# Optimization experiments

Hardware: AMD Instinct MI355X
Metric: run time of the kernel (lower is better)

Reference implementation:

```python
import jax, jax.numpy as jnp
import numpy as np

N, C, T, V, M = 256, 3, 300, 25, 2
H = 256            # sub_hidden == main_hidden
NUM_CLASS = 60
IN = C * V         # 75 = dim_point * num_joint


def _lstm(xs, Wih, Whh, bih, bhh):
    """Single-layer LSTM over (N,T,I) -> (N,T,H), zero initial state."""
    h_dim = Whh.shape[1]
    n = xs.shape[0]
    b = bih + bhh

    def step(carry, x_t):
        h, c = carry
        g = x_t @ Wih.T + h @ Whh.T + b          # (N,4H)
        i, f, gg, o = jnp.split(g, 4, axis=-1)
        c = jax.nn.sigmoid(f) * c + jax.nn.sigmoid(i) * jnp.tanh(gg)
        h = jax.nn.sigmoid(o) * jnp.tanh(c)
        return (h, c), h

    init = (jnp.zeros((n, h_dim), xs.dtype), jnp.zeros((n, h_dim), xs.dtype))
    _, hs = jax.lax.scan(step, init, jnp.swapaxes(xs, 0, 1))
    return jnp.swapaxes(hs, 0, 1)                # (N,T,H)


def _rot_mats(a):
    """Batched Rx@Ry@Rz from angles a (N,3), matching the torch formulas."""
    c, s = jnp.cos(a), jnp.sin(a)
    z = jnp.zeros_like(c[:, 0]); o = jnp.ones_like(z)
    Rx = jnp.stack([jnp.stack([o, z, z], -1),
                    jnp.stack([z,  c[:, 0], s[:, 0]], -1),
                    jnp.stack([z, -s[:, 0], c[:, 0]], -1)], -2)
    Ry = jnp.stack([jnp.stack([c[:, 1], z, -s[:, 1]], -1),
                    jnp.stack([z, o, z], -1),
                    jnp.stack([s[:, 1], z,  c[:, 1]], -1)], -2)
    Rz = jnp.stack([jnp.stack([ c[:, 2], s[:, 2], z], -1),
                    jnp.stack([-s[:, 2], c[:, 2], z], -1),
                    jnp.stack([z, z, o], -1)], -2)
    return Rx @ Ry @ Rz                           # (N,3,3)


def setup_inputs() -> dict:
    key = jax.random.key(0)
    ks = iter(jax.random.split(key, 40))
    g = lambda shape: jax.random.normal(next(ks), shape, dtype=jnp.float32) * 0.05
    inp = {"x": jax.random.normal(next(ks), (N, C, T, V, M), dtype=jnp.float32)}
    for pre, i_dim in (("rot", IN), ("tr", IN)):
        inp[pre + "_Wih"] = g((4 * H, i_dim))
        inp[pre + "_Whh"] = g((4 * H, H))
        inp[pre + "_bih"] = g((4 * H,))
        inp[pre + "_bhh"] = g((4 * H,))
        inp[pre + "_fcW"] = g((3, H))
        inp[pre + "_fcb"] = g((3,))
    for li, i_dim in ((0, IN), (1, H), (2, H)):
        inp[f"m{li}_Wih"] = g((4 * H, i_dim))
        inp[f"m{li}_Whh"] = g((4 * H, H))
        inp[f"m{li}_bih"] = g((4 * H,))
        inp[f"m{li}_bhh"] = g((4 * H,))
    inp["fcW"] = g((NUM_CLASS, H))
    inp["fcb"] = g((NUM_CLASS,))
    return inp


def reference(x,
              rot_Wih, rot_Whh, rot_bih, rot_bhh, rot_fcW, rot_fcb,
              tr_Wih, tr_Whh, tr_bih, tr_bhh, tr_fcW, tr_fcb,
              m0_Wih, m0_Whh, m0_bih, m0_bhh,
              m1_Wih, m1_Whh, m1_bih, m1_bhh,
              m2_Wih, m2_Whh, m2_bih, m2_bhh,
              fcW, fcb):
    n, c, t, v, m = x.shape

    def person_feat(xm):                          # xm: (N,C,T,V)
        seq = xm.transpose(0, 2, 1, 3).reshape(n, t, c * v)   # (N,T,CV)
        h_rot = _lstm(seq, rot_Wih, rot_Whh, rot_bih, rot_bhh)[:, -1]
        ang = (h_rot @ rot_fcW.T + rot_fcb) * jnp.pi          # (N,3)
        h_tr = _lstm(seq, tr_Wih, tr_Whh, tr_bih, tr_bhh)[:, -1]
        trans = h_tr @ tr_fcW.T + tr_fcb                      # (N,3)
        R = _rot_mats(ang)                                    # (N,3,3)
        xs = xm - trans[:, :, None, None]                     # translate
        xr = jnp.einsum('nij,njk->nik', R, xs.reshape(n, c, t * v))
        seq2 = xr.reshape(n, c, t, v).transpose(0, 2, 1, 3).reshape(n, t, c * v)
        h = _lstm(seq2, m0_Wih, m0_Whh, m0_bih, m0_bhh)
        h = _lstm(h, m1_Wih, m1_Whh, m1_bih, m1_bhh)
        h = _lstm(h, m2_Wih, m2_Whh, m2_bih, m2_bhh)
        return h[:, -1]                                       # (N,H)

    h0 = person_feat(x[..., 0])
    h1 = person_feat(x[..., 1])
    out = jnp.maximum(h0, h1)
    return out @ fcW.T + fcb                                  # (N,num_class)
```

## Files before the change

### kernel.cpp

```cpp
#include <hip/hip_runtime.h>
#include <hip/hip_fp16.h>

#define N_ 256
#define C_ 3
#define T_ 300
#define V_ 25
#define H_ 256
#define G4_ 1024
#define IN_ 75
#define XP1_ 96
#define NCLS_ 60

typedef _Float16 half_t;
typedef __attribute__((ext_vector_type(8))) _Float16 half8;
typedef __attribute__((ext_vector_type(4))) float f32x4;
typedef __attribute__((ext_vector_type(4))) unsigned int uint4v;
typedef __attribute__((ext_vector_type(2))) unsigned int uint2v;

static_assert(sizeof(half8) == 16, "half8 must be 16B");

__device__ __forceinline__ float tanh_f(float x) {
  x = fminf(fmaxf(x, -15.0f), 15.0f);
  float e = __expf(2.0f * x);
  return (e - 1.0f) / (e + 1.0f);
}

__device__ __forceinline__ half8 gload16_cc(const void* p) {
  uint4v r;
  asm volatile("global_load_dwordx4 %0, %1, off sc0 sc1" : "=v"(r) : "v"(p));
  return __builtin_bit_cast(half8, r);
}
__device__ __forceinline__ void store8_cc(void* p, uint2v v) {
  asm volatile("global_store_dwordx2 %0, %1, off sc0 sc1" :: "v"(p), "v"(v) : "memory");
}
__device__ __forceinline__ void waitvm0() {
  asm volatile("s_waitcnt vmcnt(0)" ::: "memory");
  __builtin_amdgcn_sched_barrier(0);
}

__global__ void pack_wcat(const float* __restrict__ Whh, const float* __restrict__ Wih,
                          const float* __restrict__ bih, const float* __restrict__ bhh,
                          half_t* __restrict__ dstW, float* __restrict__ dstB,
                          int inDim, int Kc) {
  int idx = blockIdx.x * 256 + threadIdx.x;
  int tot = G4_ * Kc;
  if (idx < tot) {
    int row = idx / Kc, k = idx % Kc;
    float v = 0.0f;
    if (k < H_) v = Whh[row * H_ + k];
    else if (k - H_ < inDim) v = Wih[row * inDim + (k - H_)];
    dstW[idx] = (half_t)v;
  }
  if (idx < G4_) dstB[idx] = bih[idx] + bhh[idx];
}

__global__ void pack_seq(const float* __restrict__ x, half_t* __restrict__ seqb) {
  int idx = blockIdx.x * 256 + threadIdx.x;
  const int tot = 2 * N_ * T_ * XP1_;
  if (idx >= tot) return;
  int k = idx % XP1_; int r = idx / XP1_;
  int t = r % T_; int r2 = r / T_;
  int n = r2 % N_; int p = r2 / N_;
  float v = 0.0f;
  if (k < IN_) {
    int c = k / V_, vv = k % V_;
    v = x[(((size_t)n * C_ + c) * T_ + t) * (V_ * 2) + vv * 2 + p];
  }
  seqb[idx] = (half_t)v;
}

template<int KT, bool POLLX>
__device__ __forceinline__ void run_layer(
    const half_t* __restrict__ Wcat, const float* __restrict__ bias,
    const half_t* __restrict__ xseq,
    half_t* __restrict__ ring, int rr,
    half_t* __restrict__ hseq, float* __restrict__ hlast,
    int ringRow0, int seqRow0, int u0, int member,
    half_t* hstage) {
  constexpr int XKT = KT - 8;
  constexpr int XK = XKT * 32;
  constexpr int Kc = KT * 32;
  const int tid = threadIdx.x, lane = tid & 63, wave = tid >> 6;
  const int col = lane & 15, khalf = lane >> 4, klo8 = khalf * 8, gq = col & 3;
  const int srow = tid >> 3, spart = tid & 7;

  half8 wreg[2][KT];
  float brg[2];
#pragma unroll
  for (int ntp = 0; ntp < 2; ++ntp) {
    int lrow = (wave * 2 + ntp) * 16 + col;
    int grow = (lrow & 3) * 256 + u0 + (lrow >> 2);
#pragma unroll
    for (int kt = 0; kt < KT; ++kt)
      wreg[ntp][kt] = *reinterpret_cast<const half8*>(Wcat + (size_t)grow * Kc + kt * 32 + klo8);
    brg[ntp] = bias[grow];
  }

  const half_t* xrow[2];
#pragma unroll
  for (int c = 0; c < 2; ++c)
    xrow[c] = xseq + (size_t)(seqRow0 + c * 16 + col) * T_ * XK + klo8;

  float creg[2][2][4] = {};

  auto chk = [](half8 v) -> unsigned {
    uint4v u = __builtin_bit_cast(uint4v, v);
    return ((u[0] & 0xFFFFu) == 0xFFFFu) | ((u[1] & 0xFFFFu) == 0xFFFFu) |
           ((u[2] & 0xFFFFu) == 0xFFFFu) | ((u[3] & 0xFFFFu) == 0xFFFFu);
  };

#pragma unroll 1
  for (int t = 0; t < T_; ++t) {
    const int sc_ = t % 3;
    const int sp_ = (t + 2) % 3;
    const int sn_ = (t + 1) % 3;
    const bool hasH = (t > 0);

    half8 ax[2][XKT];
    half8 ah[2][8];

    if (!POLLX) {
#pragma unroll
      for (int c = 0; c < 2; ++c)
#pragma unroll
        for (int kx = 0; kx < XKT; ++kx)
          ax[c][kx] = *reinterpret_cast<const half8*>(xrow[c] + (size_t)t * XK + kx * 32);
    }

    if (hasH || POLLX) {
      int guard = 0;
      for (;;) {
        if (hasH) {
#pragma unroll
          for (int c = 0; c < 2; ++c)
#pragma unroll
            for (int kt = 0; kt < 8; ++kt)
              ah[c][kt] = gload16_cc(
                  ring + ((size_t)(sp_ * 8 + kt) * rr + ringRow0 + c * 16 + col) * 32 + klo8);
        }
        if (POLLX) {
#pragma unroll
          for (int c = 0; c < 2; ++c)
#pragma unroll
            for (int kx = 0; kx < XKT; ++kx)
              ax[c][kx] = gload16_cc(xrow[c] + (size_t)t * XK + kx * 32);
        }
        waitvm0();
        unsigned bad = 0;
        if (hasH) {
#pragma unroll
          for (int c = 0; c < 2; ++c)
#pragma unroll
            for (int kt = 0; kt < 8; ++kt) bad |= chk(ah[c][kt]);
        }
        if (POLLX) {
#pragma unroll
          for (int c = 0; c < 2; ++c)
#pragma unroll
            for (int kx = 0; kx < XKT; ++kx) bad |= chk(ax[c][kx]);
        }
        if (__all(bad == 0u)) break;
        if (++guard > (1 << 20)) break;
        __builtin_amdgcn_s_sleep(1);
      }
      __syncthreads();
      __builtin_amdgcn_sched_barrier(0);
    }

    {
      uint2v sent = {0xFFFFFFFFu, 0xFFFFFFFFu};
      store8_cc(ring + ((size_t)(sn_ * 8 + member) * rr + ringRow0 + srow) * 32 + spart * 4, sent);
    }

#pragma unroll
    for (int c = 0; c < 2; ++c) {
      f32x4 acc[2];
      acc[0] = (f32x4){brg[0], brg[0], brg[0], brg[0]};
      acc[1] = (f32x4){brg[1], brg[1], brg[1], brg[1]};
      if (hasH) {
#pragma unroll
        for (int kt = 0; kt < 8; ++kt) {
          acc[0] = __builtin_amdgcn_mfma_f32_16x16x32_f16(ah[c][kt], wreg[0][kt], acc[0], 0, 0, 0);
          acc[1] = __builtin_amdgcn_mfma_f32_16x16x32_f16(ah[c][kt], wreg[1][kt], acc[1], 0, 0, 0);
        }
      }
#pragma unroll
      for (int kx = 0; kx < XKT; ++kx) {
        acc[0] = __builtin_amdgcn_mfma_f32_16x16x32_f16(ax[c][kx], wreg[0][8 + kx], acc[0], 0, 0, 0);
        acc[1] = __builtin_amdgcn_mfma_f32_16x16x32_f16(ax[c][kx], wreg[1][8 + kx], acc[1], 0, 0, 0);
      }
#pragma unroll
      for (int ntp = 0; ntp < 2; ++ntp) {
        int nt = wave * 2 + ntp;
        int ul = nt * 4 + (col >> 2);
#pragma unroll
        for (int r = 0; r < 4; ++r) {
          float v = acc[ntp][r];
          float y = (gq == 2) ? 2.0f * v : v;
          float s = 1.0f / (1.0f + __expf(-y));
          float av = (gq == 2) ? (2.0f * s - 1.0f) : s;
          float b1v = __shfl_xor(av, 1);
          float b2v = __shfl_xor(av, 2);
          float b3v = __shfl_xor(b1v, 2);
          auto pick = [&](int k2) { return k2 == 0 ? av : (k2 == 1 ? b1v : (k2 == 2 ? b2v : b3v)); };
          float iv = pick(gq), fv = pick(gq ^ 1), gv = pick(gq ^ 2), ov = pick(gq ^ 3);
          float cc = fv * creg[c][ntp][r] + iv * gv;
          creg[c][ntp][r] = cc;
          float h = ov * tanh_f(cc);
          if (gq == 0) {
            int s_ = c * 16 + khalf * 4 + r;
            hstage[s_ * 32 + ul] = (half_t)h;
            if (hlast != nullptr && t == T_ - 1)
              hlast[(size_t)(seqRow0 + s_) * H_ + u0 + ul] = h;
          }
        }
      }
    }
    __syncthreads();

    waitvm0();
    {
      uint2v val = *reinterpret_cast<const uint2v*>(&hstage[srow * 32 + spart * 4]);
      store8_cc(ring + ((size_t)(sc_ * 8 + member) * rr + ringRow0 + srow) * 32 + spart * 4, val);
      if (hseq)
        store8_cc(&hseq[((size_t)(seqRow0 + srow) * T_ + t) * H_ + u0 + spart * 4], val);
    }
  }
}

__global__ __launch_bounds__(256, 1) void lstm_p1(
    const half_t* __restrict__ W0, const half_t* __restrict__ W1,
    const float* __restrict__ b0, const float* __restrict__ b1,
    const half_t* __restrict__ xseq, half_t* __restrict__ ring,
    float* __restrict__ hl0, float* __restrict__ hl1) {
  __shared__ __align__(8) half_t hstage[32 * 32];
  const int member = blockIdx.x >> 5;
  const int g = blockIdx.x & 31;
  const int run = g >> 4;
  run_layer<11, false>(run ? W1 : W0, run ? b1 : b0, xseq,
                       ring, 1024, nullptr, run ? hl1 : hl0,
                       g * 32, g * 32 - run * 512, member * 32, member, hstage);
}

template<int KT, bool POLLX>
__device__ __forceinline__ void ml_layer(
    const half_t* __restrict__ Wcat, const float* __restrict__ bias,
    const half_t* __restrict__ xseq,
    half_t* __restrict__ ring,
    half_t* __restrict__ hseq, float* __restrict__ hlast,
    unsigned int* __restrict__ ownf, const unsigned int* __restrict__ upf,
    int seqRow0, int u0, int member,
    half_t* hstage) {
  constexpr int XKT = KT - 8;
  constexpr int XK = XKT * 32;
  constexpr int Kc = KT * 32;
  const int tid = threadIdx.x, lane = tid & 63, wave = tid >> 6;
  const int w4 = wave & 3, chalf = wave >> 2;
  const int col = lane & 15, khalf = lane >> 4, klo8 = khalf * 8, gq = col & 3;
  const int srow = tid >> 3, spart = tid & 7;

  half8 wreg[2][KT];
  float brg[2];
#pragma unroll
  for (int ntp = 0; ntp < 2; ++ntp) {
    int lrow = (w4 * 2 + ntp) * 16 + col;
    int grow = (lrow & 3) * 256 + u0 + (lrow >> 2);
#pragma unroll
    for (int kt = 0; kt < KT; ++kt)
      wreg[ntp][kt] = *reinterpret_cast<const half8*>(Wcat + (size_t)grow * Kc + kt * 32 + klo8);
    brg[ntp] = bias[grow];
  }

  const half_t* xrow[2];
#pragma unroll
  for (int c = 0; c < 2; ++c)
    xrow[c] = xseq + (size_t)(seqRow0 + (chalf * 2 + c) * 16 + col) * T_ * XK + klo8;

  float creg[2][2][4] = {};

#pragma unroll 1
  for (int t = 0; t < T_; ++t) {
    const bool hasH = (t > 0);

    if (wave == 0) {
      const unsigned tgt = (lane < 8) ? (unsigned)t : (unsigned)(t + 1);
      const unsigned int* fp = (lane < 8) ? (ownf + lane) : (upf + (lane - 8));
      const bool act = (lane < 8) ? (t > 0) : (POLLX && lane < 16);
      int guard = 0;
      for (;;) {
        unsigned f = 0xFFFFFFFFu;
        if (act) f = __hip_atomic_load(fp, __ATOMIC_RELAXED, __HIP_MEMORY_SCOPE_AGENT);
        if (__all(f >= tgt)) break;
        if (++guard > (1 << 22)) break;
        __builtin_amdgcn_s_sleep(2);
      }
    }
    __syncthreads();
    __builtin_amdgcn_sched_barrier(0);

#pragma unroll
    for (int c = 0; c < 2; ++c) {
      const int cc = chalf * 2 + c;
      half8 ah[8];
      half8 ax[XKT];
      if (hasH) {
#pragma unroll
        for (int kt = 0; kt < 8; ++kt)
          ah[kt] = gload16_cc(
              ring + ((size_t)(((t - 1) & 1) * 8 + kt) * 512 + seqRow0 + cc * 16 + col) * 32 + klo8);
      }
      if (POLLX) {
#pragma unroll
        for (int kx = 0; kx < XKT; ++kx)
          ax[kx] = gload16_cc(xrow[c] + (size_t)t * XK + kx * 32);
      } else {
#pragma unroll
        for (int kx = 0; kx < XKT; ++kx)
          ax[kx] = *reinterpret_cast<const half8*>(xrow[c] + (size_t)t * XK + kx * 32);
      }
      waitvm0();

      f32x4 acc[2];
      acc[0] = (f32x4){brg[0], brg[0], brg[0], brg[0]};
      acc[1] = (f32x4){brg[1], brg[1], brg[1], brg[1]};
      if (hasH) {
#pragma unroll
        for (int kt = 0; kt < 8; ++kt) {
          acc[0] = __builtin_amdgcn_mfma_f32_16x16x32_f16(ah[kt], wreg[0][kt], acc[0], 0, 0, 0);
          acc[1] = __builtin_amdgcn_mfma_f32_16x16x32_f16(ah[kt], wreg[1][kt], acc[1], 0, 0, 0);
        }
      }
#pragma unroll
      for (int kx = 0; kx < XKT; ++kx) {
        acc[0] = __builtin_amdgcn_mfma_f32_16x16x32_f16(ax[kx], wreg[0][8 + kx], acc[0], 0, 0, 0);
        acc[1] = __builtin_amdgcn_mfma_f32_16x16x32_f16(ax[kx], wreg[1][8 + kx], acc[1], 0, 0, 0);
      }
#pragma unroll
      for (int ntp = 0; ntp < 2; ++ntp) {
        int nt = w4 * 2 + ntp;
        int ul = nt * 4 + (col >> 2);
#pragma unroll
        for (int r = 0; r < 4; ++r) {
          float v = acc[ntp][r];
          float y = (gq == 2) ? 2.0f * v : v;
          float s = 1.0f / (1.0f + __expf(-y));
          float av = (gq == 2) ? (2.0f * s - 1.0f) : s;
          float b1v = __shfl_xor(av, 1);
          float b2v = __shfl_xor(av, 2);
          float b3v = __shfl_xor(b1v, 2);
          auto pick = [&](int k2) { return k2 == 0 ? av : (k2 == 1 ? b1v : (k2 == 2 ? b2v : b3v)); };
          float iv = pick(gq), fv = pick(gq ^ 1), gv = pick(gq ^ 2), ov = pick(gq ^ 3);
          float ccv = fv * creg[c][ntp][r] + iv * gv;
          creg[c][ntp][r] = ccv;
          float h = ov * tanh_f(ccv);
          if (gq == 0) {
            int s_ = cc * 16 + khalf * 4 + r;
            hstage[s_ * 32 + ul] = (half_t)h;
            if (hlast != nullptr && t == T_ - 1)
              hlast[(size_t)(seqRow0 + s_) * H_ + u0 + ul] = h;
          }
        }
      }
    }
    __syncthreads();

    {
      uint2v val = *reinterpret_cast<const uint2v*>(&hstage[srow * 32 + spart * 4]);
      store8_cc(ring + ((size_t)((t & 1) * 8 + member) * 512 + seqRow0 + srow) * 32 + spart * 4, val);
      if (hseq)
        store8_cc(&hseq[((size_t)(seqRow0 + srow) * T_ + t) * H_ + u0 + spart * 4], val);
    }
    waitvm0();
    __syncthreads();
    if (tid == 0)
      __hip_atomic_fetch_add(ownf + member, 1u, __ATOMIC_RELAXED, __HIP_MEMORY_SCOPE_AGENT);
  }
}

__global__ __launch_bounds__(512, 1) void lstm_ml512(
    const half_t* __restrict__ Wm0, const float* __restrict__ Bm0,
    const half_t* __restrict__ Wm1, const float* __restrict__ Bm1,
    const half_t* __restrict__ Wm2, const float* __restrict__ Bm2,
    const half_t* __restrict__ seqb, half_t* __restrict__ hs0, half_t* __restrict__ hs1,
    half_t* __restrict__ ring0, half_t* __restrict__ ring1, half_t* __restrict__ ring2,
    unsigned int* __restrict__ flags, float* __restrict__ hlast2) {
  __shared__ __align__(8) half_t hstage[64 * 32];
  const int L = blockIdx.x / 64;
  const int r = blockIdx.x % 64;
  const int member = r >> 3;
  const int g = r & 7;
  const int seqRow0 = g * 64, u0 = member * 32;
  unsigned int* ownf = flags + (L * 8 + g) * 32;
  const unsigned int* upf = (L > 0) ? (flags + ((L - 1) * 8 + g) * 32) : flags;
  if (L == 0)
    ml_layer<11, false>(Wm0, Bm0, seqb, ring0, hs0, nullptr, ownf, upf, seqRow0, u0, member, hstage);
  else if (L == 1)
    ml_layer<16, true>(Wm1, Bm1, hs0, ring1, hs1, nullptr, ownf, upf, seqRow0, u0, member, hstage);
  else
    ml_layer<16, true>(Wm2, Bm2, hs1, ring2, nullptr, hlast2, ownf, upf, seqRow0, u0, member, hstage);
}

__global__ void fc3_rot(const float* __restrict__ hrot, const float* __restrict__ htr,
                        const float* __restrict__ rfcW, const float* __restrict__ rfcb,
                        const float* __restrict__ tfcW, const float* __restrict__ tfcb,
                        float* __restrict__ rt) {
  int idx = blockIdx.x * blockDim.x + threadIdx.x;
  if (idx >= 2 * N_) return;
  const float* h1 = hrot + (size_t)idx * H_;
  const float* h2 = htr + (size_t)idx * H_;
  float ang[3], tr[3];
#pragma unroll
  for (int i = 0; i < 3; ++i) {
    float a = rfcb[i], b = tfcb[i];
    for (int j = 0; j < H_; ++j) { a += h1[j] * rfcW[i * H_ + j]; b += h2[j] * tfcW[i * H_ + j]; }
    ang[i] = a * 3.14159265358979323846f;
    tr[i] = b;
  }
  float c0 = cosf(ang[0]), s0 = sinf(ang[0]);
  float c1 = cosf(ang[1]), s1 = sinf(ang[1]);
  float c2 = cosf(ang[2]), s2 = sinf(ang[2]);
  float Rx[3][3] = {{1, 0, 0}, {0, c0, s0}, {0, -s0, c0}};
  float Ry[3][3] = {{c1, 0, -s1}, {0, 1, 0}, {s1, 0, c1}};
  float Rz[3][3] = {{c2, s2, 0}, {-s2, c2, 0}, {0, 0, 1}};
  float A[3][3], R[3][3];
  for (int i = 0; i < 3; ++i)
    for (int j = 0; j < 3; ++j) {
      float s = 0;
      for (int k = 0; k < 3; ++k) s += Rx[i][k] * Ry[k][j];
      A[i][j] = s;
    }
  for (int i = 0; i < 3; ++i)
    for (int j = 0; j < 3; ++j) {
      float s = 0;
      for (int k = 0; k < 3; ++k) s += A[i][k] * Rz[k][j];
      R[i][j] = s;
    }
  float* o = rt + (size_t)idx * 12;
  for (int i = 0; i < 9; ++i) o[i] = R[i / 3][i % 3];
  for (int i = 0; i < 3; ++i) o[9 + i] = tr[i];
}

__global__ void transform_seq(const float* __restrict__ x, const float* __restrict__ rt,
                              half_t* __restrict__ seqb) {
  int idx = blockIdx.x * 256 + threadIdx.x;
  const int tot = 2 * N_ * T_ * V_;
  if (idx >= tot) return;
  int v = idx % V_; int r = idx / V_;
  int t = r % T_; int r2 = r / T_;
  int n = r2 % N_; int p = r2 / N_;
  const float* o = rt + ((size_t)p * N_ + n) * 12;
  float xv[3];
#pragma unroll
  for (int c = 0; c < 3; ++c)
    xv[c] = x[(((size_t)n * C_ + c) * T_ + t) * (V_ * 2) + v * 2 + p] - o[9 + c];
  size_t base = (((size_t)p * N_ + n) * T_ + t) * XP1_;
#pragma unroll
  for (int i = 0; i < 3; ++i) {
    float s = o[i * 3 + 0] * xv[0] + o[i * 3 + 1] * xv[1] + o[i * 3 + 2] * xv[2];
    seqb[base + i * V_ + v] = (half_t)s;
  }
}

__global__ void final_fc(const float* __restrict__ hM2, const float* __restrict__ fcW,
                         const float* __restrict__ fcb, float* __restrict__ out) {
  int n = blockIdx.x;
  __shared__ float hm[H_];
  for (int j = threadIdx.x; j < H_; j += blockDim.x)
    hm[j] = fmaxf(hM2[(size_t)n * H_ + j], hM2[(size_t)(N_ + n) * H_ + j]);
  __syncthreads();
  if (threadIdx.x < NCLS_) {
    float acc = fcb[threadIdx.x];
    for (int j = 0; j < H_; ++j) acc += hm[j] * fcW[threadIdx.x * H_ + j];
    out[n * NCLS_ + threadIdx.x] = acc;
  }
}

extern "C" void kernel_launch(void* const* d_in, const int* in_sizes, int n_in,
                              void* d_out, int out_size, void* d_ws, size_t ws_size,
                              hipStream_t stream) {
  const float* x       = (const float*)d_in[0];
  const float* rot_Wih = (const float*)d_in[1];
  const float* rot_Whh = (const float*)d_in[2];
  const float* rot_bih = (const float*)d_in[3];
  const float* rot_bhh = (const float*)d_in[4];
  const float* rot_fcW = (const float*)d_in[5];
  const float* rot_fcb = (const float*)d_in[6];
  const float* tr_Wih  = (const float*)d_in[7];
  const float* tr_Whh  = (const float*)d_in[8];
  const float* tr_bih  = (const float*)d_in[9];
  const float* tr_bhh  = (const float*)d_in[10];
  const float* tr_fcW  = (const float*)d_in[11];
  const float* tr_fcb  = (const float*)d_in[12];
  const float* m0_Wih  = (const float*)d_in[13];
  const float* m0_Whh  = (const float*)d_in[14];
  const float* m0_bih  = (const float*)d_in[15];
  const float* m0_bhh  = (const float*)d_in[16];
  const float* m1_Wih  = (const float*)d_in[17];
  const float* m1_Whh  = (const float*)d_in[18];
  const float* m1_bih  = (const float*)d_in[19];
  const float* m1_bhh  = (const float*)d_in[20];
  const float* m2_Wih  = (const float*)d_in[21];
  const float* m2_Whh  = (const float*)d_in[22];
  const float* m2_bih  = (const float*)d_in[23];
  const float* m2_bhh  = (const float*)d_in[24];
  const float* fcW     = (const float*)d_in[25];
  const float* fcb     = (const float*)d_in[26];

  char* ws = (char*)d_ws;
  size_t off = 0;
  auto take = [&](size_t b) -> void* {
    void* pp = ws + off;
    off = (off + b + 255) & ~(size_t)255;
    return pp;
  };
  half_t* WC_ROT = (half_t*)take((size_t)G4_ * 352 * 2);
  half_t* WC_TR  = (half_t*)take((size_t)G4_ * 352 * 2);
  half_t* WC_M0  = (half_t*)take((size_t)G4_ * 352 * 2);
  half_t* WC_M1  = (half_t*)take((size_t)G4_ * 512 * 2);
  half_t* WC_M2  = (half_t*)take((size_t)G4_ * 512 * 2);
  float* B_ROT = (float*)take((size_t)G4_ * 4);
  float* B_TR  = (float*)take((size_t)G4_ * 4);
  float* B_M0  = (float*)take((size_t)G4_ * 4);
  float* B_M1  = (float*)take((size_t)G4_ * 4);
  float* B_M2  = (float*)take((size_t)G4_ * 4);
  half_t* SEQB = (half_t*)take((size_t)2 * N_ * T_ * XP1_ * 2);
  float* HL_ROT = (float*)take((size_t)2 * N_ * H_ * 4);
  float* HL_TR  = (float*)take((size_t)2 * N_ * H_ * 4);
  float* HL_M2  = (float*)take((size_t)2 * N_ * H_ * 4);
  float* RT     = (float*)take((size_t)2 * N_ * 12 * 4);
  half_t* RINGP  = (half_t*)take((size_t)3 * 8 * 1024 * 32 * 2);
  half_t* RINGM0 = (half_t*)take((size_t)2 * 8 * 512 * 32 * 2);
  half_t* RINGM1 = (half_t*)take((size_t)2 * 8 * 512 * 32 * 2);
  half_t* RINGM2 = (half_t*)take((size_t)2 * 8 * 512 * 32 * 2);
  unsigned int* FLAGS = (unsigned int*)take((size_t)24 * 32 * sizeof(unsigned int));
  half_t* HS0 = (half_t*)take((size_t)2 * N_ * T_ * H_ * 2);
  half_t* HS1 = (half_t*)take((size_t)2 * N_ * T_ * H_ * 2);

  hipMemsetAsync(RINGP, 0xFF, (size_t)3 * 8 * 1024 * 32 * 2, stream);
  hipMemsetAsync(FLAGS, 0, (size_t)24 * 32 * sizeof(unsigned int), stream);

  pack_wcat<<<1408, 256, 0, stream>>>(rot_Whh, rot_Wih, rot_bih, rot_bhh, WC_ROT, B_ROT, IN_, 352);
  pack_wcat<<<1408, 256, 0, stream>>>(tr_Whh, tr_Wih, tr_bih, tr_bhh, WC_TR, B_TR, IN_, 352);
  pack_wcat<<<1408, 256, 0, stream>>>(m0_Whh, m0_Wih, m0_bih, m0_bhh, WC_M0, B_M0, IN_, 352);
  pack_wcat<<<2048, 256, 0, stream>>>(m1_Whh, m1_Wih, m1_bih, m1_bhh, WC_M1, B_M1, H_, 512);
  pack_wcat<<<2048, 256, 0, stream>>>(m2_Whh, m2_Wih, m2_bih, m2_bhh, WC_M2, B_M2, H_, 512);

  pack_seq<<<(2 * N_ * T_ * XP1_ + 255) / 256, 256, 0, stream>>>(x, SEQB);

  lstm_p1<<<256, 256, 0, stream>>>(WC_ROT, WC_TR, B_ROT, B_TR, SEQB, RINGP, HL_ROT, HL_TR);

  fc3_rot<<<2, 256, 0, stream>>>(HL_ROT, HL_TR, rot_fcW, rot_fcb, tr_fcW, tr_fcb, RT);
  transform_seq<<<(2 * N_ * T_ * V_ + 255) / 256, 256, 0, stream>>>(x, RT, SEQB);

  lstm_ml512<<<192, 512, 0, stream>>>(
      WC_M0, B_M0, WC_M1, B_M1, WC_M2, B_M2,
      SEQB, HS0, HS1, RINGM0, RINGM1, RINGM2, FLAGS, HL_M2);

  final_fc<<<256, 64, 0, stream>>>(HL_M2, fcW, fcb, (float*)d_out);
}
```

Before: 6.802 ms.

## Stage recurrent and layer-input tiles through swizzled LDS with time-major hidden sequences

Each timestep, every wave now loads one slice of the previous hidden state from the ring, and of the upstream layer output, with contiguous per-row loads. These are written into XOR-swizzled LDS buffers, and the MFMA operands are read from LDS. Before, each wave fetched scattered 16-byte fragments from global memory, and both CU halves loaded the same data twice. The intermediate hidden sequences change to time-major layout so a timestep's rows are contiguous. Layer-0 inputs are prefetched before the flag poll. The added barrier and 64KB of LDS per block, plus the launch_bounds change to 2, may affect occupancy and register allocation.

```diff
diff --git a/kernel.cpp b/kernel.cpp
--- a/kernel.cpp
+++ b/kernel.cpp
@@ -250,7 +250,7 @@
     half_t* __restrict__ hseq, float* __restrict__ hlast,
     unsigned int* __restrict__ ownf, const unsigned int* __restrict__ upf,
     int seqRow0, int u0, int member,
-    half_t* hstage) {
+    half_t* hlds, half_t* xlds, half_t* hstage) {
   constexpr int XKT = KT - 8;
   constexpr int XK = XKT * 32;
   constexpr int Kc = KT * 32;
@@ -272,9 +272,11 @@
   }
 
   const half_t* xrow[2];
-#pragma unroll
-  for (int c = 0; c < 2; ++c)
-    xrow[c] = xseq + (size_t)(seqRow0 + (chalf * 2 + c) * 16 + col) * T_ * XK + klo8;
+  if (!POLLX) {
+#pragma unroll
+    for (int c = 0; c < 2; ++c)
+      xrow[c] = xseq + (size_t)(seqRow0 + (chalf * 2 + c) * 16 + col) * T_ * XK + klo8;
+  }
 
   float creg[2][2][4] = {};
 
@@ -282,10 +284,19 @@
   for (int t = 0; t < T_; ++t) {
     const bool hasH = (t > 0);
 
+    half8 axd[2][XKT];
+    if (!POLLX) {
+#pragma unroll
+      for (int c = 0; c < 2; ++c)
+#pragma unroll
+        for (int kx = 0; kx < XKT; ++kx)
+          axd[c][kx] = *reinterpret_cast<const half8*>(xrow[c] + (size_t)t * XK + kx * 32);
+    }
+
     if (wave == 0) {
       const unsigned tgt = (lane < 8) ? (unsigned)t : (unsigned)(t + 1);
+      const bool act = (lane < 8) ? (t > 0) : (POLLX && lane < 16);
       const unsigned int* fp = (lane < 8) ? (ownf + lane) : (upf + (lane - 8));
-      const bool act = (lane < 8) ? (t > 0) : (POLLX && lane < 16);
       int guard = 0;
       for (;;) {
         unsigned f = 0xFFFFFFFFu;
@@ -298,42 +309,59 @@
     __syncthreads();
     __builtin_amdgcn_sched_barrier(0);
 
+    {
+      const int r = lane;
+      half8 hv[4], xv[4];
+      if (hasH) {
+        const half_t* src = ring + ((size_t)(((t - 1) & 1) * 8 + wave) * 512 + seqRow0 + r) * 32;
+#pragma unroll
+        for (int j = 0; j < 4; ++j) hv[j] = gload16_cc(src + j * 8);
+      }
+      if (POLLX) {
+        const half_t* sx = xseq + ((size_t)t * 512 + seqRow0 + r) * 256 + wave * 32;
+#pragma unroll
+        for (int j = 0; j < 4; ++j) xv[j] = gload16_cc(sx + j * 8);
+      }
+      waitvm0();
+      if (hasH) {
+#pragma unroll
+        for (int j = 0; j < 4; ++j)
+          *reinterpret_cast<half8*>(&hlds[r * 256 + 8 * ((wave * 4 + j) ^ (r & 31))]) = hv[j];
+      }
+      if (POLLX) {
+#pragma unroll
+        for (int j = 0; j < 4; ++j)
+          *reinterpret_cast<half8*>(&xlds[r * 256 + 8 * ((wave * 4 + j) ^ (r & 31))]) = xv[j];
+      }
+    }
+    __syncthreads();
+
 #pragma unroll
     for (int c = 0; c < 2; ++c) {
       const int cc = chalf * 2 + c;
-      half8 ah[8];
-      half8 ax[XKT];
-      if (hasH) {
-#pragma unroll
-        for (int kt = 0; kt < 8; ++kt)
-          ah[kt] = gload16_cc(
-              ring + ((size_t)(((t - 1) & 1) * 8 + kt) * 512 + seqRow0 + cc * 16 + col) * 32 + klo8);
-      }
-      if (POLLX) {
-#pragma unroll
-        for (int kx = 0; kx < XKT; ++kx)
-          ax[kx] = gload16_cc(xrow[c] + (size_t)t * XK + kx * 32);
-      } else {
-#pragma unroll
-        for (int kx = 0; kx < XKT; ++kx)
-          ax[kx] = *reinterpret_cast<const half8*>(xrow[c] + (size_t)t * XK + kx * 32);
-      }
-      waitvm0();
-
+      const int row = cc * 16 + col;
       f32x4 acc[2];
       acc[0] = (f32x4){brg[0], brg[0], brg[0], brg[0]};
       acc[1] = (f32x4){brg[1], brg[1], brg[1], brg[1]};
       if (hasH) {
 #pragma unroll
         for (int kt = 0; kt < 8; ++kt) {
-          acc[0] = __builtin_amdgcn_mfma_f32_16x16x32_f16(ah[kt], wreg[0][kt], acc[0], 0, 0, 0);
-          acc[1] = __builtin_amdgcn_mfma_f32_16x16x32_f16(ah[kt], wreg[1][kt], acc[1], 0, 0, 0);
+          half8 ah = *reinterpret_cast<const half8*>(
+              &hlds[row * 256 + 8 * ((kt * 4 + khalf) ^ (row & 31))]);
+          acc[0] = __builtin_amdgcn_mfma_f32_16x16x32_f16(ah, wreg[0][kt], acc[0], 0, 0, 0);
+          acc[1] = __builtin_amdgcn_mfma_f32_16x16x32_f16(ah, wreg[1][kt], acc[1], 0, 0, 0);
         }
       }
 #pragma unroll
       for (int kx = 0; kx < XKT; ++kx) {
-        acc[0] = __builtin_amdgcn_mfma_f32_16x16x32_f16(ax[kx], wreg[0][8 + kx], acc[0], 0, 0, 0);
-        acc[1] = __builtin_amdgcn_mfma_f32_16x16x32_f16(ax[kx], wreg[1][8 + kx], acc[1], 0, 0, 0);
+        half8 ax;
+        if (POLLX)
+          ax = *reinterpret_cast<const half8*>(
+              &xlds[row * 256 + 8 * ((kx * 4 + khalf) ^ (row & 31))]);
+        else
+          ax = axd[c][kx];
+        acc[0] = __builtin_amdgcn_mfma_f32_16x16x32_f16(ax, wreg[0][8 + kx], acc[0], 0, 0, 0);
+        acc[1] = __builtin_amdgcn_mfma_f32_16x16x32_f16(ax, wreg[1][8 + kx], acc[1], 0, 0, 0);
       }
 #pragma unroll
       for (int ntp = 0; ntp < 2; ++ntp) {
@@ -368,7 +396,7 @@
       uint2v val = *reinterpret_cast<const uint2v*>(&hstage[srow * 32 + spart * 4]);
       store8_cc(ring + ((size_t)((t & 1) * 8 + member) * 512 + seqRow0 + srow) * 32 + spart * 4, val);
       if (hseq)
-        store8_cc(&hseq[((size_t)(seqRow0 + srow) * T_ + t) * H_ + u0 + spart * 4], val);
+        store8_cc(&hseq[((size_t)t * 512 + seqRow0 + srow) * 256 + u0 + spart * 4], val);
     }
     waitvm0();
     __syncthreads();
@@ -377,14 +405,16 @@
   }
 }
 
-__global__ __launch_bounds__(512, 1) void lstm_ml512(
+__global__ __launch_bounds__(512, 2) void lstm_ml512(
     const half_t* __restrict__ Wm0, const float* __restrict__ Bm0,
     const half_t* __restrict__ Wm1, const float* __restrict__ Bm1,
     const half_t* __restrict__ Wm2, const float* __restrict__ Bm2,
     const half_t* __restrict__ seqb, half_t* __restrict__ hs0, half_t* __restrict__ hs1,
     half_t* __restrict__ ring0, half_t* __restrict__ ring1, half_t* __restrict__ ring2,
     unsigned int* __restrict__ flags, float* __restrict__ hlast2) {
-  __shared__ __align__(8) half_t hstage[64 * 32];
+  __shared__ __align__(16) half_t hlds[64 * 256];
+  __shared__ __align__(16) half_t xlds[64 * 256];
+  __shared__ __align__(8)  half_t hstage[64 * 32];
   const int L = blockIdx.x / 64;
   const int r = blockIdx.x % 64;
   const int member = r >> 3;
@@ -393,11 +423,14 @@
   unsigned int* ownf = flags + (L * 8 + g) * 32;
   const unsigned int* upf = (L > 0) ? (flags + ((L - 1) * 8 + g) * 32) : flags;
   if (L == 0)
-    ml_layer<11, false>(Wm0, Bm0, seqb, ring0, hs0, nullptr, ownf, upf, seqRow0, u0, member, hstage);
+    ml_layer<11, false>(Wm0, Bm0, seqb, ring0, hs0, nullptr, ownf, upf, seqRow0, u0, member,
+                        hlds, xlds, hstage);
   else if (L == 1)
-    ml_layer<16, true>(Wm1, Bm1, hs0, ring1, hs1, nullptr, ownf, upf, seqRow0, u0, member, hstage);
+    ml_layer<16, true>(Wm1, Bm1, hs0, ring1, hs1, nullptr, ownf, upf, seqRow0, u0, member,
+                       hlds, xlds, hstage);
   else
-    ml_layer<16, true>(Wm2, Bm2, hs1, ring2, nullptr, hlast2, ownf, upf, seqRow0, u0, member, hstage);
+    ml_layer<16, true>(Wm2, Bm2, hs1, ring2, nullptr, hlast2, ownf, upf, seqRow0, u0, member,
+                       hlds, xlds, hstage);
 }
 
 __global__ void fc3_rot(const float* __restrict__ hrot, const float* __restrict__ htr,
@@ -533,8 +566,8 @@
   half_t* RINGM1 = (half_t*)take((size_t)2 * 8 * 512 * 32 * 2);
   half_t* RINGM2 = (half_t*)take((size_t)2 * 8 * 512 * 32 * 2);
   unsigned int* FLAGS = (unsigned int*)take((size_t)24 * 32 * sizeof(unsigned int));
-  half_t* HS0 = (half_t*)take((size_t)2 * N_ * T_ * H_ * 2);
-  half_t* HS1 = (half_t*)take((size_t)2 * N_ * T_ * H_ * 2);
+  half_t* HS0 = (half_t*)take((size_t)T_ * 512 * H_ * 2);
+  half_t* HS1 = (half_t*)take((size_t)T_ * 512 * H_ * 2);
 
   hipMemsetAsync(RINGP, 0xFF, (size_t)3 * 8 * 1024 * 32 * 2, stream);
   hipMemsetAsync(FLAGS, 0, (size_t)24 * 32 * sizeof(unsigned int), stream);
```

Measured after the change: 6.375 ms. 6.3% less time.
